# Kernel optimization log

Hardware: AMD Instinct MI355X
Metric: run time of the kernel (lower is better)

Reference implementation:

```python
import jax, jax.numpy as jnp
import numpy as np

B, T, C, Y = 16, 8192, 512, 256
MAX_DUR = 64

def setup_inputs() -> dict:
    key = jax.random.key(0)
    k1, k2 = jax.random.split(key)
    emg_feats = jax.random.normal(k1, (B, T, C), dtype=jnp.float32)
    durations = jax.random.randint(k2, (B, Y), 0, MAX_DUR, dtype=jnp.int32)
    return {"emg_feats": emg_feats, "durations": durations}

def _pool_by_durations(emg_feats, durations):
    # Faithful vectorized version of EMG2PhonemeAligner.pool_by_durations
    # (durations_in_mel=False path: durs_emg = durations).
    # For each phoneme span [start, end) (clamped to [0, T]), take the mean of
    # the EMG frames in that span; empty spans produce zeros.
    Bs, Ts, Cs = emg_feats.shape
    Ys = durations.shape[1]
    cum = jnp.cumsum(durations, axis=1)                      # (B, Y) exclusive ends
    starts = cum - durations                                 # (B, Y)
    # segment id of each frame t: first phoneme whose cumulative end exceeds t.
    # Frames past the total duration land in overflow bucket Y (dropped).
    t = jnp.arange(Ts)
    ids = jax.vmap(lambda c: jnp.searchsorted(c, t, side='right'))(cum)  # (B, T)
    seg_sum = jax.vmap(
        lambda f, i: jax.ops.segment_sum(f, i, num_segments=Ys + 1)
    )(emg_feats, ids)[:, :Ys]                                # (B, Y, C)
    s = jnp.clip(starts, 0, Ts)
    e = jnp.clip(cum, 0, Ts)
    cnt = (e - s).astype(emg_feats.dtype)                    # (B, Y) frames per span
    mean = seg_sum / jnp.maximum(cnt, 1)[..., None]
    return jnp.where(cnt[..., None] > 0, mean, jnp.zeros((), emg_feats.dtype))

def reference(emg_feats, durations):
    return _pool_by_durations(emg_feats, durations)
```

## Files before the change

### kernel.cpp

```cpp
#include <hip/hip_runtime.h>

#define BB 16
#define TT 8192
#define CC 512
#define YY 256
#define C4 128

__global__ __launch_bounds__(256) void emg_pool_kernel(
    const float* __restrict__ emg,
    const int*   __restrict__ dur,
    float*       __restrict__ out)
{
    const int y   = blockIdx.x;
    const int b   = blockIdx.y;
    const int tid = threadIdx.x;

    const int* drow = dur + b * YY;
    int v = (tid < y) ? drow[tid] : 0;
    #pragma unroll
    for (int off = 32; off > 0; off >>= 1) v += __shfl_down(v, off, 64);
    __shared__ int partial[4];
    if ((tid & 63) == 0) partial[tid >> 6] = v;
    __syncthreads();
    const int s   = partial[0] + partial[1] + partial[2] + partial[3];
    const int e   = s + drow[y];
    const int sc  = (s < TT) ? s : TT;
    const int ec  = (e < TT) ? e : TT;
    const int cnt = ec - sc;

    const int c4 = tid & (C4 - 1);
    const int fo = tid >> 7;
    const float4* src = (const float4*)emg + (size_t)b * TT * C4 + c4;

    float4 acc = make_float4(0.f, 0.f, 0.f, 0.f);
    #pragma unroll 4
    for (int t = sc + fo; t < ec; t += 2) {
        float4 x = src[(size_t)t * C4];
        acc.x += x.x; acc.y += x.y; acc.z += x.z; acc.w += x.w;
    }

    __shared__ float4 red[C4];
    if (fo == 1) red[c4] = acc;
    __syncthreads();
    if (fo == 0) {
        float4 o = make_float4(0.f, 0.f, 0.f, 0.f);
        if (cnt > 0) {
            const float inv = 1.0f / (float)cnt;
            const float4 r = red[c4];
            o.x = (acc.x + r.x) * inv;
            o.y = (acc.y + r.y) * inv;
            o.z = (acc.z + r.z) * inv;
            o.w = (acc.w + r.w) * inv;
        }
        ((float4*)out)[((size_t)b * YY + y) * C4 + c4] = o;
    }
}

extern "C" void kernel_launch(void* const* d_in, const int* in_sizes, int n_in,
                              void* d_out, int out_size, void* d_ws, size_t ws_size,
                              hipStream_t stream) {
    const float* emg = (const float*)d_in[0];
    const int*   dur = (const int*)d_in[1];
    float*       out = (float*)d_out;

    dim3 grid(YY, BB);
    emg_pool_kernel<<<grid, 256, 0, stream>>>(emg, dur, out);
}
```

Before: 360.0 us.

## Split pooling into scan, frame-chunked atomic accumulation, and finalize kernels

Replaces the one-block-per-segment kernel with three kernels. The first zeroes a workspace sum and prefix-scans durations. The second assigns fixed 64-frame chunks to blocks and atomically adds partial segment sums. The third divides by the counts. This targets load imbalance, since segment lengths vary and many frames fall beyond the segments, at the cost of atomics, extra launches and workspace traffic.

```diff
diff --git a/kernel.cpp b/kernel.cpp
--- a/kernel.cpp
+++ b/kernel.cpp
@@ -1,59 +1,110 @@
 #include <hip/hip_runtime.h>
+
 
 #define BB 16
 #define TT 8192
 #define CC 512
 #define YY 256
 #define C4 128
+#define FPB 64
+#define NCHUNK (TT / FPB)
 
-__global__ __launch_bounds__(256) void emg_pool_kernel(
-    const float* __restrict__ emg,
-    const int*   __restrict__ dur,
-    float*       __restrict__ out)
+__global__ __launch_bounds__(256) void init_scan_kernel(
+    float4* __restrict__ sum4, const int* __restrict__ dur,
+    int* __restrict__ cum, int* __restrict__ cnt)
 {
-    const int y   = blockIdx.x;
-    const int b   = blockIdx.y;
     const int tid = threadIdx.x;
+    const size_t i = (size_t)blockIdx.x * 256 + tid;
+    sum4[i] = make_float4(0.f, 0.f, 0.f, 0.f);
 
-    const int* drow = dur + b * YY;
-    int v = (tid < y) ? drow[tid] : 0;
-    #pragma unroll
-    for (int off = 32; off > 0; off >>= 1) v += __shfl_down(v, off, 64);
-    __shared__ int partial[4];
-    if ((tid & 63) == 0) partial[tid >> 6] = v;
+    if (blockIdx.x < BB) {
+        const int b = blockIdx.x;
+        __shared__ int sc[YY];
+        const int d = dur[b * YY + tid];
+        sc[tid] = d;
+        for (int off = 1; off < YY; off <<= 1) {
+            __syncthreads();
+            const int add = (tid >= off) ? sc[tid - off] : 0;
+            __syncthreads();
+            sc[tid] += add;
+        }
+        const int c  = sc[tid];
+        const int s  = c - d;
+        const int ec = (c < TT) ? c : TT;
+        const int scl = (s < TT) ? s : TT;
+        cum[b * YY + tid] = c;
+        cnt[b * YY + tid] = ec - scl;
+    }
+}
+
+__global__ __launch_bounds__(256) void accumulate_kernel(
+    const float4* __restrict__ emg4, const int* __restrict__ cum,
+    float* __restrict__ sum)
+{
+    const int tid = threadIdx.x;
+    const int b  = blockIdx.y;
+    const int f0 = blockIdx.x * FPB;
+    const int f1 = f0 + FPB;
+
+    __shared__ int cum_s[YY];
+    cum_s[tid] = cum[b * YY + tid];
     __syncthreads();
-    const int s   = partial[0] + partial[1] + partial[2] + partial[3];
-    const int e   = s + drow[y];
-    const int sc  = (s < TT) ? s : TT;
-    const int ec  = (e < TT) ? e : TT;
-    const int cnt = ec - sc;
+
+    int lo_i = 0, hi_i = YY;
+    while (lo_i < hi_i) {
+        const int m = (lo_i + hi_i) >> 1;
+        if (cum_s[m] <= f0) lo_i = m + 1; else hi_i = m;
+    }
+    int y = lo_i;
 
     const int c4 = tid & (C4 - 1);
     const int fo = tid >> 7;
-    const float4* src = (const float4*)emg + (size_t)b * TT * C4 + c4;
+    const float4* src = emg4 + (size_t)b * TT * C4 + c4;
+    __shared__ float4 red[C4];
 
-    float4 acc = make_float4(0.f, 0.f, 0.f, 0.f);
-    #pragma unroll 4
-    for (int t = sc + fo; t < ec; t += 2) {
-        float4 x = src[(size_t)t * C4];
-        acc.x += x.x; acc.y += x.y; acc.z += x.z; acc.w += x.w;
+    int lo = f0;
+    while (y < YY && lo < f1) {
+        int hi = cum_s[y]; if (hi > f1) hi = f1;
+
+        float4 acc = make_float4(0.f, 0.f, 0.f, 0.f);
+        #pragma unroll 4
+        for (int t = lo + fo; t < hi; t += 2) {
+            const float4 x = src[(size_t)t * C4];
+            acc.x += x.x; acc.y += x.y; acc.z += x.z; acc.w += x.w;
+        }
+
+        __syncthreads();
+        if (fo == 1) red[c4] = acc;
+        __syncthreads();
+        if (fo == 0) {
+            const float4 r = red[c4];
+            float* dst = sum + ((size_t)(b * YY + y)) * CC + c4 * 4;
+            atomicAdd(dst + 0, acc.x + r.x);
+            atomicAdd(dst + 1, acc.y + r.y);
+            atomicAdd(dst + 2, acc.z + r.z);
+            atomicAdd(dst + 3, acc.w + r.w);
+        }
+
+        lo = hi;
+        y++;
+        while (y < YY && cum_s[y] <= lo) y++;
     }
+}
 
-    __shared__ float4 red[C4];
-    if (fo == 1) red[c4] = acc;
-    __syncthreads();
-    if (fo == 0) {
-        float4 o = make_float4(0.f, 0.f, 0.f, 0.f);
-        if (cnt > 0) {
-            const float inv = 1.0f / (float)cnt;
-            const float4 r = red[c4];
-            o.x = (acc.x + r.x) * inv;
-            o.y = (acc.y + r.y) * inv;
-            o.z = (acc.z + r.z) * inv;
-            o.w = (acc.w + r.w) * inv;
-        }
-        ((float4*)out)[((size_t)b * YY + y) * C4 + c4] = o;
+__global__ __launch_bounds__(256) void finalize_kernel(
+    const float4* __restrict__ sum4, const int* __restrict__ cnt,
+    float4* __restrict__ out4)
+{
+    const size_t i = (size_t)blockIdx.x * 256 + threadIdx.x;
+    const int by = (int)(i >> 7);
+    const int c  = cnt[by];
+    const float4 s = sum4[i];
+    float4 o = make_float4(0.f, 0.f, 0.f, 0.f);
+    if (c > 0) {
+        const float inv = 1.0f / (float)c;
+        o.x = s.x * inv; o.y = s.y * inv; o.z = s.z * inv; o.w = s.w * inv;
     }
+    out4[i] = o;
 }
 
 extern "C" void kernel_launch(void* const* d_in, const int* in_sizes, int n_in,
@@ -63,6 +114,13 @@
     const int*   dur = (const int*)d_in[1];
     float*       out = (float*)d_out;
 
-    dim3 grid(YY, BB);
-    emg_pool_kernel<<<grid, 256, 0, stream>>>(emg, dur, out);
+    float* ws_sum = (float*)d_ws;
+    int*   ws_cum = (int*)((char*)d_ws + ((size_t)8 << 20));
+    int*   ws_cnt = ws_cum + BB * YY;
+
+    init_scan_kernel<<<2048, 256, 0, stream>>>((float4*)ws_sum, dur, ws_cum, ws_cnt);
+    accumulate_kernel<<<dim3(NCHUNK, BB), 256, 0, stream>>>(
+        (const float4*)emg, ws_cum, ws_sum);
+    finalize_kernel<<<2048, 256, 0, stream>>>(
+        (const float4*)ws_sum, ws_cnt, (float4*)out);
 }
```

Result: slower. 369.5 us (+2.6%).
